# Kernel optimization log

Measured on AMD Instinct MI355X. Metric: run time of the kernel, lower is better.

## Reference

```python
import jax, jax.numpy as jnp
import numpy as np
import math

B, H, W, C = 8, 112, 112, 192
WS, SHIFT, NH = 7, 3, 6
HD = C // NH
N = WS * WS
NW = (H // WS) * (W // WS)
MLP_HID = 4 * C
LOG100 = math.log(100.0)


def _rel_table():
    ch = np.arange(-(WS - 1), WS, dtype=np.float32)
    t = np.stack(np.meshgrid(ch, ch, indexing='ij')).transpose(1, 2, 0).reshape(-1, 2)
    t = t / float(WS - 1) * 8.0
    t = np.sign(t) * np.log2(np.abs(t) + 1.0) / np.log2(8.0)
    return t.astype(np.float32)  # ((2*WS-1)^2, 2)


def _rel_index():
    coords = np.stack(np.meshgrid(np.arange(WS), np.arange(WS), indexing='ij')).reshape(2, -1)
    rel = (coords[:, :, None] - coords[:, None, :]).transpose(1, 2, 0)
    rel = rel + np.array([WS - 1, WS - 1])
    rel = rel * np.array([2 * WS - 1, 1])
    return rel.sum(-1).astype(np.int32)  # (N, N)


def _attn_mask():
    img = np.zeros((H, W), dtype=np.float32)
    cnt = 0
    for hsl in (slice(0, -WS), slice(-WS, -SHIFT), slice(-SHIFT, None)):
        for wsl in (slice(0, -WS), slice(-WS, -SHIFT), slice(-SHIFT, None)):
            img[hsl, wsl] = cnt
            cnt += 1
    mw = img.reshape(H // WS, WS, W // WS, WS).transpose(0, 2, 1, 3).reshape(-1, N)
    diff = mw[:, None, :] - mw[:, :, None]
    return np.where(diff != 0, -100.0, 0.0).astype(np.float32)  # (NW, N, N)

REL_TABLE = jnp.asarray(_rel_table())
REL_INDEX = jnp.asarray(_rel_index())
ATTN_MASK = jnp.asarray(_attn_mask())


def _ln(v, g, b, eps=1e-5):
    m = jnp.mean(v, axis=-1, keepdims=True)
    s = jnp.mean((v - m) ** 2, axis=-1, keepdims=True)
    return (v - m) / jnp.sqrt(s + eps) * g + b


def setup_inputs() -> dict:
    key = jax.random.key(0)
    ks = jax.random.split(key, 12)
    std = 0.02
    inp = {
        'x': jax.random.normal(ks[0], (B, H * W, C), jnp.float32),
        'q_w': jax.random.normal(ks[1], (C, C), jnp.float32) * std,
        'q_b': jnp.zeros((C,), jnp.float32),
        'k_w': jax.random.normal(ks[2], (C, C), jnp.float32) * std,
        'v_w': jax.random.normal(ks[3], (C, C), jnp.float32) * std,
        'v_b': jnp.zeros((C,), jnp.float32),
        'proj_w': jax.random.normal(ks[4], (C, C), jnp.float32) * std,
        'proj_b': jnp.zeros((C,), jnp.float32),
        'logit_scale': jnp.log(10.0 * jnp.ones((NH, 1, 1), jnp.float32)),
        'cpb_w0': jax.random.normal(ks[5], (2, 512), jnp.float32) * std,
        'cpb_b0': jnp.zeros((512,), jnp.float32),
        'cpb_w1': jax.random.normal(ks[6], (512, NH), jnp.float32) * std,
        'ln1_g': jnp.ones((C,), jnp.float32),
        'ln1_b': jnp.zeros((C,), jnp.float32),
        'ln2_g': jnp.ones((C,), jnp.float32),
        'ln2_b': jnp.zeros((C,), jnp.float32),
        'fc1_w': jax.random.normal(ks[7], (C, MLP_HID), jnp.float32) * std,
        'fc1_b': jnp.zeros((MLP_HID,), jnp.float32),
        'fc2_w': jax.random.normal(ks[8], (MLP_HID, C), jnp.float32) * std,
        'fc2_b': jnp.zeros((C,), jnp.float32),
    }
    return inp


def reference(x, q_w, q_b, k_w, v_w, v_b, proj_w, proj_b, logit_scale,
              cpb_w0, cpb_b0, cpb_w1, ln1_g, ln1_b, ln2_g, ln2_b,
              fc1_w, fc1_b, fc2_w, fc2_b):
    shortcut = x  # (B, L, C)
    h = x.reshape(B, H, W, C)
    # cyclic shift
    h = jnp.roll(h, shift=(-SHIFT, -SHIFT), axis=(1, 2))
    # window partition -> (B*NW, N, C)
    h = h.reshape(B, H // WS, WS, W // WS, WS, C).transpose(0, 1, 3, 2, 4, 5)
    h = h.reshape(B * NW, N, C)

    q = (h @ q_w + q_b).reshape(-1, N, NH, HD).transpose(0, 2, 1, 3)
    k = (h @ k_w).reshape(-1, N, NH, HD).transpose(0, 2, 1, 3)
    v = (h @ v_w + v_b).reshape(-1, N, NH, HD).transpose(0, 2, 1, 3)

    # cosine-similarity attention
    q = q / jnp.maximum(jnp.linalg.norm(q, axis=-1, keepdims=True), 1e-6)
    k = k / jnp.maximum(jnp.linalg.norm(k, axis=-1, keepdims=True), 1e-6)
    scale = jnp.exp(jnp.minimum(logit_scale, LOG100))  # (NH,1,1)
    attn = jnp.einsum('bhqd,bhkd->bhqk', q, k) * scale

    # relative position bias via CPB MLP
    rpb = jax.nn.relu(REL_TABLE @ cpb_w0 + cpb_b0) @ cpb_w1  # (169, NH)
    rpb = rpb[REL_INDEX.reshape(-1)].reshape(N, N, NH).transpose(2, 0, 1)
    rpb = 16.0 * jax.nn.sigmoid(rpb)  # (NH, N, N)
    attn = attn + rpb[None]

    # shift mask
    attn = attn.reshape(B, NW, NH, N, N) + ATTN_MASK[None, :, None]
    attn = attn.reshape(B * NW, NH, N, N)
    attn = jax.nn.softmax(attn, axis=-1)

    out = jnp.einsum('bhqk,bhkd->bhqd', attn, v)
    out = out.transpose(0, 2, 1, 3).reshape(B * NW, N, C)
    out = out @ proj_w + proj_b

    # window reverse + reverse shift
    out = out.reshape(B, H // WS, W // WS, WS, WS, C).transpose(0, 1, 3, 2, 4, 5)
    out = out.reshape(B, H, W, C)
    out = jnp.roll(out, shift=(SHIFT, SHIFT), axis=(1, 2)).reshape(B, H * W, C)

    # post-norm residual (Swin-v2)
    h1 = shortcut + _ln(out, ln1_g, ln1_b)
    mlp = jax.nn.gelu(h1 @ fc1_w + fc1_b) @ fc2_w + fc2_b
    return h1 + _ln(mlp, ln2_g, ln2_b)
```

## Files before the change

### kernel.cpp

```cpp
#include <hip/hip_runtime.h>

typedef unsigned short u16;
typedef unsigned int   u32;
typedef __attribute__((ext_vector_type(8))) short bf16x8;
typedef __attribute__((ext_vector_type(4))) float f32x4;

#define B_      8
#define HW_     112
#define C_      192
#define NH_     6
#define HD_     32
#define L_      (HW_*HW_)
#define M_      (B_*L_)
#define MLP_    768
#define QKVN_   576
#define LOG100_ 4.6051702f
#define LOG2E_  1.44269504f

__device__ __forceinline__ float bf2f(u16 u){
  union { float f; u32 i; } v; v.i = ((u32)u) << 16; return v.f;
}
__device__ __forceinline__ u16 f2bf(float f){
  union { float f; u32 i; } v; v.f = f;
  u32 r = (v.i + 0x7fffu + ((v.i >> 16) & 1u)) >> 16;
  return (u16)r;
}
__device__ __forceinline__ u32 cvtpk(float a, float b){
  u32 r;
  asm("v_cvt_pk_bf16_f32 %0, %1, %2" : "=v"(r) : "v"(a), "v"(b));
  return r;
}
__device__ __forceinline__ void u4_to_f8(uint4 u, float* f){
  f[0]=bf2f((u16)(u.x&0xffffu)); f[1]=bf2f((u16)(u.x>>16));
  f[2]=bf2f((u16)(u.y&0xffffu)); f[3]=bf2f((u16)(u.y>>16));
  f[4]=bf2f((u16)(u.z&0xffffu)); f[5]=bf2f((u16)(u.z>>16));
  f[6]=bf2f((u16)(u.w&0xffffu)); f[7]=bf2f((u16)(u.w>>16));
}

__device__ __forceinline__ int rowelem(int b, int wh, int ww, int t){
  int i = t/7, j = t - i*7;
  int oi = wh*7 + i + 3; if (oi >= 112) oi -= 112;
  int oj = ww*7 + j + 3; if (oj >= 112) oj -= 112;
  return b*L_ + oi*112 + oj;
}

__global__ __launch_bounds__(256) void prep_weights(
    const float* __restrict__ qw, const float* __restrict__ qb,
    const float* __restrict__ kw, const float* __restrict__ vw,
    const float* __restrict__ vb, const float* __restrict__ pw,
    const float* __restrict__ pb, const float* __restrict__ f1w,
    const float* __restrict__ f1b, const float* __restrict__ f2w,
    const float* __restrict__ f2b,
    u16* __restrict__ wt_qkv, float* __restrict__ b_qkv,
    u16* __restrict__ wt_p,   float* __restrict__ b_p,
    u16* __restrict__ wt_f1,  float* __restrict__ b_f1,
    u16* __restrict__ wt_f2,  float* __restrict__ b_f2)
{
  const int S1 = 110592, S2 = 147456, S3 = 294912, S4 = 442368, TOT = 444096;
  int i = blockIdx.x*256 + threadIdx.x;
  if (i >= TOT) return;
  if (i < S1) {
    int n = i/192, k = i%192;
    float v = (n<192) ? qw[k*192+n] : ((n<384) ? kw[k*192+(n-192)] : vw[k*192+(n-384)]);
    wt_qkv[i] = f2bf(v);
  } else if (i < S2) {
    int j = i - S1; int n = j/192, k = j%192;
    wt_p[j] = f2bf(pw[k*192+n]);
  } else if (i < S3) {
    int j = i - S2; int n = j/192, k = j%192;
    wt_f1[j] = f2bf(f1w[k*768+n]);
  } else if (i < S4) {
    int j = i - S3; int n = j/768, k = j%768;
    wt_f2[j] = f2bf(f2w[k*192+n]);
  } else {
    int j = i - S4;
    if (j < 576)        b_qkv[j] = (j<192) ? qb[j] : ((j<384) ? 0.f : vb[j-384]);
    else if (j < 768)   b_p[j-576]   = pb[j-576];
    else if (j < 1536)  b_f1[j-768]  = f1b[j-768];
    else                b_f2[j-1536] = f2b[j-1536];
  }
}

__device__ __forceinline__ float reltab(float x){
  float v = x * (8.f/6.f);
  float r = __log2f(fabsf(v) + 1.f) * (1.f/3.f);
  return (v < 0.f) ? -r : r;
}

__global__ __launch_bounds__(64) void rpb_a_kernel(
    const float* __restrict__ w0, const float* __restrict__ b0,
    const float* __restrict__ w1, float* __restrict__ rpb169)
{
  int tt = blockIdx.x, lane = threadIdx.x;
  float t0 = reltab((float)(tt/13 - 6));
  float t1 = reltab((float)(tt%13 - 6));
  float acc[6] = {0.f,0.f,0.f,0.f,0.f,0.f};
  for (int j = lane; j < 512; j += 64){
    float hid = fmaxf(t0*w0[j] + t1*w0[512+j] + b0[j], 0.f);
#pragma unroll
    for (int h=0; h<6; h++) acc[h] += hid * w1[j*6+h];
  }
#pragma unroll
  for (int h=0; h<6; h++){
#pragma unroll
    for (int m=32; m>=1; m>>=1) acc[h] += __shfl_xor(acc[h], m);
  }
  if (lane == 0){
#pragma unroll
    for (int h=0; h<6; h++) rpb169[tt*6+h] = acc[h];
  }
}

__global__ __launch_bounds__(256) void rpb_b_kernel(
    const float* __restrict__ rpb169, float* __restrict__ biasQ)
{
  int i = blockIdx.x*256 + threadIdx.x;
  if (i >= 98304) return;
  int j = i & 63, q = (i >> 6) & 63;
  int rest = i >> 12;
  int hh = rest % 6, type = rest / 6;
  int kt = j >> 4, s = j & 15;
  int key = ((kt>>1)<<5) + ((s>>2)<<3) + ((kt&1)<<2) + (s&3);
  float val;
  if (key >= 49) val = -60000.f;
  else if (q >= 49) val = 0.f;
  else {
    int qi = q/7, qj = q%7, ki = key/7, kj = key%7;
    int idx = (qi - ki + 6)*13 + (qj - kj + 6);
    float x = rpb169[idx*6 + hh];
    float sig = 16.f / (1.f + __expf(-x));
    int th = type >> 1, tw = type & 1;
    int rq = (th ? (qi<4?1:2) : 0)*3 + (tw ? (qj<4?1:2) : 0);
    int rk = (th ? (ki<4?1:2) : 0)*3 + (tw ? (kj<4?1:2) : 0);
    float msk = (rq != rk) ? -100.f : 0.f;
    val = (sig + msk) * LOG2E_;
  }
  biasQ[i] = val;
}

__device__ __forceinline__ float fast_gelu(float v){
  float t = v*v;
  float w = v * fmaf(-0.1029432f, t, -2.30220817f);
  float e = exp2f(w);
  return v * __builtin_amdgcn_rcpf(1.f + e);
}

#define MODE_GELU 0
#define MODE_LN1  1
#define MODE_LN2  2

template<int K, int MODE>
__global__ __launch_bounds__(512,4) void gemm_fused(
    const u16* __restrict__ A, const u16* __restrict__ Wt,
    const float* __restrict__ bias,
    const float* __restrict__ lng, const float* __restrict__ lnb,
    const float* __restrict__ base32, const u16* __restrict__ base16,
    u16* __restrict__ out16, float* __restrict__ out32, int NN)
{
  __shared__ __align__(16) u16 lds[20480];
  const int tid  = threadIdx.x;
  const int wave = tid >> 6, lane = tid & 63;
  const int m0 = blockIdx.x * 128;
  const int n0 = blockIdx.y * 192;
  const int wr = wave >> 1, wc = wave & 1;
  const int lrow = lane >> 2, lslot = lane & 3;
  const int gk = (lslot ^ ((lrow >> 1) & 3)) * 8;

  const u16* gsrc[3]; u32 ldst[3]; const int nst = (wave < 4) ? 3 : 2;
#pragma unroll
  for (int t=0; t<3; t++){
    int c = wave + t*8;
    if (c < 8)       { gsrc[t] = A  + (size_t)(m0 + c*16 + lrow)*K + gk;      ldst[t] = (u32)(c*512); }
    else if (c < 20) { gsrc[t] = Wt + (size_t)(n0 + (c-8)*16 + lrow)*K + gk;  ldst[t] = (u32)(4096 + (c-8)*512); }
    else             { gsrc[t] = A; ldst[t] = 0; }
  }
  const int lr16 = lane & 15;
  const int lg   = lane >> 4;
  const int slot8 = (lg ^ ((lr16 >> 1) & 3)) * 8;
  u32 aoff[2], boff[6];
#pragma unroll
  for (int mt=0; mt<2; mt++) aoff[mt] = (u32)((wr*32 + mt*16 + lr16)*32 + slot8);
#pragma unroll
  for (int nt=0; nt<6; nt++) boff[nt] = (u32)(4096 + (wc*96 + nt*16 + lr16)*32 + slot8);

  f32x4 acc[2][6];
#pragma unroll
  for (int mt=0; mt<2; mt++)
#pragma unroll
    for (int nt=0; nt<6; nt++)
      acc[mt][nt] = (f32x4){0.f,0.f,0.f,0.f};

  const int NT = K/32;
#define STAGE_F(tt, ph) do { \
  _Pragma("unroll") \
  for (int s_=0; s_<3; s_++) if (s_ < nst) \
    __builtin_amdgcn_global_load_lds( \
        (const __attribute__((address_space(1))) void*)(gsrc[s_] + (tt)*32), \
        (__attribute__((address_space(3))) void*)&lds[ldst[s_] + (ph)], 16, 0, 0); \
} while(0)

  STAGE_F(0, 0u);
  __syncthreads();
  for (int t=0; t<NT; t++){
    const u32 pb = (u32)(t&1)*10240u;
    if (t+1 < NT) STAGE_F(t+1, pb ^ 10240u);
    bf16x8 af[2], bf[6];
#pragma unroll
    for (int mt=0; mt<2; mt++) af[mt] = *(const bf16x8*)&lds[pb + aoff[mt]];
#pragma unroll
    for (int nt=0; nt<6; nt++) bf[nt] = *(const bf16x8*)&lds[pb + boff[nt]];
#pragma unroll
    for (int mt=0; mt<2; mt++)
#pragma unroll
      for (int nt=0; nt<6; nt++)
        acc[mt][nt] = __builtin_amdgcn_mfma_f32_16x16x32_bf16(af[mt], bf[nt], acc[mt][nt], 0, 0, 0);
    __syncthreads();
  }
#undef STAGE_F

#pragma unroll
  for (int nt=0; nt<6; nt++){
    float bsv = bias[n0 + wc*96 + nt*16 + lr16];
#pragma unroll
    for (int mt=0; mt<2; mt++)
#pragma unroll
      for (int r2=0; r2<4; r2++) acc[mt][nt][r2] += bsv;
  }

  if (MODE == MODE_GELU){
#pragma unroll
    for (int mt=0; mt<2; mt++){
      int rbase = m0 + wr*32 + mt*16 + lg*4;
#pragma unroll
      for (int nt=0; nt<6; nt++){
        int col = n0 + wc*96 + nt*16 + lr16;
#pragma unroll
        for (int r2=0; r2<4; r2++)
          out16[(size_t)(rbase + r2)*NN + col] = f2bf(fast_gelu(acc[mt][nt][r2]));
      }
    }
  } else {
    float sv[2][4], sq[2][4];
#pragma unroll
    for (int mt=0; mt<2; mt++)
#pragma unroll
      for (int r2=0; r2<4; r2++){
        float s=0.f, q=0.f;
#pragma unroll
        for (int nt=0; nt<6; nt++){ float x = acc[mt][nt][r2]; s += x; q += x*x; }
        sv[mt][r2]=s; sq[mt][r2]=q;
      }
#pragma unroll
    for (int d=1; d<16; d<<=1){
#pragma unroll
      for (int mt=0; mt<2; mt++)
#pragma unroll
        for (int r2=0; r2<4; r2++){
          sv[mt][r2] += __shfl_xor(sv[mt][r2], d);
          sq[mt][r2] += __shfl_xor(sq[mt][r2], d);
        }
    }
    float* red = (float*)lds;
    if (lr16 == 0){
#pragma unroll
      for (int mt=0; mt<2; mt++)
#pragma unroll
        for (int r2=0; r2<4; r2++){
          int row = wr*32 + mt*16 + lg*4 + r2;
          red[row*4 + wc*2]     = sv[mt][r2];
          red[row*4 + wc*2 + 1] = sq[mt][r2];
        }
    }
    __syncthreads();
    float mean[2][4], rstd[2][4];
#pragma unroll
    for (int mt=0; mt<2; mt++)
#pragma unroll
      for (int r2=0; r2<4; r2++){
        int row = wr*32 + mt*16 + lg*4 + r2;
        float s = red[row*4] + red[row*4+2];
        float q = red[row*4+1] + red[row*4+3];
        float m = s*(1.f/192.f);
        float v = fmaxf(q*(1.f/192.f) - m*m, 0.f);
        mean[mt][r2] = m; rstd[mt][r2] = rsqrtf(v + 1e-5f);
      }
    float gg[6], be[6];
#pragma unroll
    for (int nt=0; nt<6; nt++){
      int col = n0 + wc*96 + nt*16 + lr16;
      gg[nt] = lng[col]; be[nt] = lnb[col];
    }
#pragma unroll
    for (int mt=0; mt<2; mt++){
      int rbase = m0 + wr*32 + mt*16 + lg*4;
#pragma unroll
      for (int nt=0; nt<6; nt++){
        int col = n0 + wc*96 + nt*16 + lr16;
#pragma unroll
        for (int r2=0; r2<4; r2++){
          size_t idx = (size_t)(rbase + r2)*192 + col;
          float r = (acc[mt][nt][r2] - mean[mt][r2])*rstd[mt][r2]*gg[nt] + be[nt];
          if (MODE == MODE_LN1){
            r += base32[idx];
            out16[idx] = f2bf(r);
          } else {
            r += bf2f(base16[idx]);
            out32[idx] = r;
          }
        }
      }
    }
  }
}

__global__ __launch_bounds__(512,4) void gemm_qkv_kernel(
    const float* __restrict__ X, const u16* __restrict__ Wt,
    const float* __restrict__ bias, u16* __restrict__ out)
{
  __shared__ __align__(16) u16 lds[20480];
  const int tid  = threadIdx.x;
  const int wave = tid >> 6, lane = tid & 63;
  const int m0 = blockIdx.x * 128;
  const int n0 = blockIdx.y * 192;
  const int wr = wave >> 1, wc = wave & 1;
  const int lrow = lane >> 2, lslot = lane & 3;
  const int gk = (lslot ^ ((lrow >> 1) & 3)) * 8;

  const u16* gsrcB[2]; u32 ldstB[2]; const int nstB = (wave < 4) ? 2 : 1;
#pragma unroll
  for (int t=0; t<2; t++){
    int c = wave + t*8;
    if (c < 12) { gsrcB[t] = Wt + (size_t)(n0 + c*16 + lrow)*192 + gk; ldstB[t] = (u32)(4096 + c*512); }
    else        { gsrcB[t] = Wt; ldstB[t] = 0; }
  }
  const int ar = tid >> 2, as = tid & 3;
  const float* gA = X + (size_t)(m0 + ar)*192 + as*8;
  const u32 dsta = (u32)(ar*32 + (as ^ ((ar >> 1) & 3))*8);

  const int lr16 = lane & 15;
  const int lg   = lane >> 4;
  const int slot8 = (lg ^ ((lr16 >> 1) & 3)) * 8;
  u32 aoff[2], boff[6];
#pragma unroll
  for (int mt=0; mt<2; mt++) aoff[mt] = (u32)((wr*32 + mt*16 + lr16)*32 + slot8);
#pragma unroll
  for (int nt=0; nt<6; nt++) boff[nt] = (u32)(4096 + (wc*96 + nt*16 + lr16)*32 + slot8);

  f32x4 acc[2][6];
#pragma unroll
  for (int mt=0; mt<2; mt++)
#pragma unroll
    for (int nt=0; nt<6; nt++)
      acc[mt][nt] = (f32x4){0.f,0.f,0.f,0.f};

#define STAGE_B(tt, ph) do { \
  _Pragma("unroll") \
  for (int s_=0; s_<2; s_++) if (s_ < nstB) \
    __builtin_amdgcn_global_load_lds( \
        (const __attribute__((address_space(1))) void*)(gsrcB[s_] + (tt)*32), \
        (__attribute__((address_space(3))) void*)&lds[ldstB[s_] + (ph)], 16, 0, 0); \
} while(0)

  {
    float4 a0 = *(const float4*)gA;
    float4 a1 = *(const float4*)(gA + 4);
    STAGE_B(0, 0u);
    uint4 aw;
    aw.x = cvtpk(a0.x, a0.y); aw.y = cvtpk(a0.z, a0.w);
    aw.z = cvtpk(a1.x, a1.y); aw.w = cvtpk(a1.z, a1.w);
    *(uint4*)(void*)&lds[dsta] = aw;
  }
  __syncthreads();

  for (int t=0; t<6; t++){
    const u32 pb = (u32)(t&1)*10240u;
    const u32 pn = pb ^ 10240u;
    float4 a0, a1;
    if (t < 5){
      a0 = *(const float4*)(gA + (t+1)*32);
      a1 = *(const float4*)(gA + (t+1)*32 + 4);
      STAGE_B(t+1, pn);
    }
    bf16x8 af[2], bf[6];
#pragma unroll
    for (int mt=0; mt<2; mt++) af[mt] = *(const bf16x8*)&lds[pb + aoff[mt]];
#pragma unroll
    for (int nt=0; nt<6; nt++) bf[nt] = *(const bf16x8*)&lds[pb + boff[nt]];
#pragma unroll
    for (int mt=0; mt<2; mt++)
#pragma unroll
      for (int nt=0; nt<6; nt++)
        acc[mt][nt] = __builtin_amdgcn_mfma_f32_16x16x32_bf16(af[mt], bf[nt], acc[mt][nt], 0, 0, 0);
    if (t < 5){
      uint4 aw;
      aw.x = cvtpk(a0.x, a0.y); aw.y = cvtpk(a0.z, a0.w);
      aw.z = cvtpk(a1.x, a1.y); aw.w = cvtpk(a1.z, a1.w);
      *(uint4*)(void*)&lds[pn + dsta] = aw;
    }
    __syncthreads();
  }
#undef STAGE_B

#pragma unroll
  for (int mt=0; mt<2; mt++){
    int rbase = m0 + wr*32 + mt*16 + lg*4;
#pragma unroll
    for (int nt=0; nt<6; nt++){
      int col = n0 + wc*96 + nt*16 + lr16;
      float bsv = bias[col];
#pragma unroll
      for (int r2=0; r2<4; r2++)
        out[(size_t)(rbase + r2)*QKVN_ + col] = f2bf(acc[mt][nt][r2] + bsv);
    }
  }
}

__global__ __launch_bounds__(64) void attn_kernel(
    const u16* __restrict__ qkv, const float* __restrict__ lsc,
    const float* __restrict__ biasQ, u16* __restrict__ attn_out)
{
  __shared__ __align__(16) u16 smem[2048];
  char* smb = (char*)smem;
  const int id = blockIdx.x;
  const int hh = id % 6;
  const int w  = id / 6;
  const int b  = w >> 8;
  const int wh = (w >> 4) & 15, ww = w & 15;
  const int lane = threadIdx.x;
  const int lg = lane >> 4, lr = lane & 15;
  const int type = ((wh==15)?2:0) + ((ww==15)?1:0);
  const float qscale = __expf(fminf(lsc[hh], LOG100_)) * LOG2E_;

  union BU { bf16x8 v; u32 u[4]; };

  const int myrow = rowelem(b, wh, ww, min(lane, 48));

  const u16* vsrc = qkv + (size_t)myrow*QKVN_ + 384 + hh*32;
  uint4 vld[4];
#pragma unroll
  for (int r=0; r<4; r++) vld[r] = *(const uint4*)(vsrc + r*8);

  int rowq[4], krow[4];
#pragma unroll
  for (int qt=0; qt<4; qt++) rowq[qt] = __shfl(myrow, qt*16 + lr);
#pragma unroll
  for (int kt=0; kt<4; kt++){
    int sig = ((kt>>1)<<5) + ((lr>>2)<<3) + ((kt&1)<<2) + (lr&3);
    krow[kt] = __shfl(myrow, sig);
  }

  bf16x8 qf[4], kf[4];
#pragma unroll
  for (int qt=0; qt<4; qt++){
    const u16* base = qkv + (size_t)rowq[qt]*QKVN_ + hh*32 + lg*8;
    uint4 u = *(const uint4*)base;
    float f[8]; u4_to_f8(u, f);
    float ss = 0.f;
#pragma unroll
    for (int d=0; d<8; d++) ss += f[d]*f[d];
    ss += __shfl_xor(ss, 16); ss += __shfl_xor(ss, 32);
    float rn = qscale * __builtin_amdgcn_rcpf(fmaxf(sqrtf(ss), 1e-6f));
    BU bu;
#pragma unroll
    for (int p=0; p<4; p++) bu.u[p] = cvtpk(f[2*p]*rn, f[2*p+1]*rn);
    qf[qt] = bu.v;
  }
#pragma unroll
  for (int kt=0; kt<4; kt++){
    const u16* base = qkv + (size_t)krow[kt]*QKVN_ + 192 + hh*32 + lg*8;
    uint4 u = *(const uint4*)base;
    float f[8]; u4_to_f8(u, f);
    float ss = 0.f;
#pragma unroll
    for (int d=0; d<8; d++) ss += f[d]*f[d];
    ss += __shfl_xor(ss, 16); ss += __shfl_xor(ss, 32);
    float rn = __builtin_amdgcn_rcpf(fmaxf(sqrtf(ss), 1e-6f));
    BU bu;
#pragma unroll
    for (int p=0; p<4; p++) bu.u[p] = cvtpk(f[2*p]*rn, f[2*p+1]*rn);
    kf[kt] = bu.v;
  }

  f32x4 s2[4][4];
#pragma unroll
  for (int kt=0; kt<4; kt++)
#pragma unroll
    for (int qt=0; qt<4; qt++)
      s2[kt][qt] = __builtin_amdgcn_mfma_f32_16x16x32_bf16(kf[kt], qf[qt],
                     (f32x4){0.f,0.f,0.f,0.f}, 0, 0, 0);

#pragma unroll
  for (int r=0; r<4; r++){
    u32 wds[4] = {vld[r].x, vld[r].y, vld[r].z, vld[r].w};
#pragma unroll
    for (int i=0; i<8; i++){
      int d = r*8 + i;
      u16 val = (u16)(wds[i>>1] >> ((i&1)*16));
      int addr = (d*128 + lane*2) ^ ((d&7)<<4);
      *(u16*)(smb + addr) = val;
    }
  }

  const float* bq = biasQ + (size_t)(type*6 + hh)*4096;
#pragma unroll
  for (int qt=0; qt<4; qt++){
    int q = qt*16 + lr;
#pragma unroll
    for (int kt=0; kt<4; kt++){
      f32x4 bv = *(const f32x4*)(bq + q*64 + kt*16 + lg*4);
      s2[kt][qt] += bv;
    }
  }
#pragma unroll
  for (int qt=0; qt<4; qt++){
    float m = s2[0][qt][0];
#pragma unroll
    for (int kt=0; kt<4; kt++)
#pragma unroll
      for (int r2=0; r2<4; r2++) m = fmaxf(m, s2[kt][qt][r2]);
    m = fmaxf(m, __shfl_xor(m, 16));
    m = fmaxf(m, __shfl_xor(m, 32));
    float sum = 0.f;
#pragma unroll
    for (int kt=0; kt<4; kt++)
#pragma unroll
      for (int r2=0; r2<4; r2++){
        float e = exp2f(s2[kt][qt][r2] - m);
        s2[kt][qt][r2] = e; sum += e;
      }
    sum += __shfl_xor(sum, 16);
    sum += __shfl_xor(sum, 32);
    float rs = __builtin_amdgcn_rcpf(sum);
#pragma unroll
    for (int kt=0; kt<4; kt++)
#pragma unroll
      for (int r2=0; r2<4; r2++) s2[kt][qt][r2] *= rs;
  }

  __syncthreads();

  f32x4 o2[2][4];
#pragma unroll
  for (int dt=0; dt<2; dt++)
#pragma unroll
    for (int qt=0; qt<4; qt++)
      o2[dt][qt] = (f32x4){0.f,0.f,0.f,0.f};

#pragma unroll
  for (int kb=0; kb<2; kb++){
    bf16x8 af[2];
#pragma unroll
    for (int dt=0; dt<2; dt++){
      int d = dt*16 + lr;
      int addr = (d*128 + kb*64 + lg*16) ^ ((d&7)<<4);
      af[dt] = *(const bf16x8*)(smb + addr);
    }
#pragma unroll
    for (int qt=0; qt<4; qt++){
      BU bu;
      bu.u[0] = cvtpk(s2[2*kb][qt][0],   s2[2*kb][qt][1]);
      bu.u[1] = cvtpk(s2[2*kb][qt][2],   s2[2*kb][qt][3]);
      bu.u[2] = cvtpk(s2[2*kb+1][qt][0], s2[2*kb+1][qt][1]);
      bu.u[3] = cvtpk(s2[2*kb+1][qt][2], s2[2*kb+1][qt][3]);
#pragma unroll
      for (int dt=0; dt<2; dt++)
        o2[dt][qt] = __builtin_amdgcn_mfma_f32_16x16x32_bf16(af[dt], bu.v, o2[dt][qt], 0, 0, 0);
    }
  }

#pragma unroll
  for (int qt=0; qt<4; qt++){
    int q = qt*16 + lr;
    if (q < 49){
      u16* op = attn_out + (size_t)rowq[qt]*C_ + hh*32;
#pragma unroll
      for (int dt=0; dt<2; dt++){
        uint2 u2;
        u2.x = cvtpk(o2[dt][qt][0], o2[dt][qt][1]);
        u2.y = cvtpk(o2[dt][qt][2], o2[dt][qt][3]);
        *(uint2*)(void*)(op + dt*16 + lg*4) = u2;
      }
    }
  }
}

__global__ __launch_bounds__(256,2) void mlp_fused_kernel(
    const u16* __restrict__ h1,
    const u16* __restrict__ wf1,
    const float* __restrict__ bf1,
    const u16* __restrict__ wf2,
    const float* __restrict__ bf2,
    const float* __restrict__ lng, const float* __restrict__ lnb,
    float* __restrict__ out)
{
  __shared__ __align__(16) char smb[75776];
  const int tid  = threadIdx.x;
  const int wave = tid >> 6, lane = tid & 63;
  const int m0 = blockIdx.x * 64;
  const int wr = wave >> 1, wc = wave & 1;
  const int lr16 = lane & 15, lg = lane >> 4;
  const int lrow = lane >> 2, lslot = lane & 3;
  const int gko = (lslot ^ ((lrow >> 1) & 3)) * 8;
  const int slot8 = (lg ^ ((lr16 >> 1) & 3)) * 8;

  {
    const u16* src = h1 + (size_t)m0*192;
#pragma unroll
    for (int j=0; j<6; j++){
      int i = tid + 256*j;
      int row = i/24, c8 = i%24;
      uint4 v = *(const uint4*)(src + i*8);
      *(uint4*)(smb + row*400 + c8*16) = v;
    }
  }

#define STG1(c_, k_, ph_) do { \
  _Pragma("unroll") \
  for (int s_=0; s_<3; s_++){ \
    int ch = wave + s_*4; \
    const u16* sp = wf1 + (size_t)((c_)*192 + ch*16 + lrow)*192 + (k_)*32 + gko; \
    __builtin_amdgcn_global_load_lds( \
        (const __attribute__((address_space(1))) void*)sp, \
        (__attribute__((address_space(3))) void*)(smb + (ph_) + ch*1024), 16, 0, 0); \
  } } while(0)
#define STG2(c_, k_, ph_) do { \
  _Pragma("unroll") \
  for (int s_=0; s_<3; s_++){ \
    int ch = wave + s_*4; \
    const u16* sp = wf2 + (size_t)(ch*16 + lrow)*768 + (c_)*192 + (k_)*32 + gko; \
    __builtin_amdgcn_global_load_lds( \
        (const __attribute__((address_space(1))) void*)sp, \
        (__attribute__((address_space(3))) void*)(smb + (ph_) + ch*1024), 16, 0, 0); \
  } } while(0)

  f32x4 oacc[2][6];
#pragma unroll
  for (int mt=0; mt<2; mt++)
#pragma unroll
    for (int nt=0; nt<6; nt++) oacc[mt][nt] = (f32x4){0.f,0.f,0.f,0.f};

  for (int c=0; c<4; c++){
    f32x4 macc[2][6];
#pragma unroll
    for (int mt=0; mt<2; mt++)
#pragma unroll
      for (int nt=0; nt<6; nt++) macc[mt][nt] = (f32x4){0.f,0.f,0.f,0.f};

    STG1(c, 0, 51200u);
    __syncthreads();
    for (int k=0; k<6; k++){
      u32 pb = 51200u + (u32)(k&1)*12288u;
      if (k < 5) STG1(c, k+1, 51200u + (u32)((k+1)&1)*12288u);
      bf16x8 af[2], bf[6];
#pragma unroll
      for (int mt=0; mt<2; mt++)
        af[mt] = *(const bf16x8*)(smb + ((wr*32 + mt*16 + lr16)*200 + k*32 + lg*8)*2);
#pragma unroll
      for (int nt=0; nt<6; nt++)
        bf[nt] = *(const bf16x8*)(smb + pb + ((wc*96 + nt*16 + lr16)*32 + slot8)*2);
#pragma unroll
      for (int mt=0; mt<2; mt++)
#pragma unroll
        for (int nt=0; nt<6; nt++)
          macc[mt][nt] = __builtin_amdgcn_mfma_f32_16x16x32_bf16(af[mt], bf[nt], macc[mt][nt], 0, 0, 0);
      __syncthreads();
    }
#pragma unroll
    for (int nt=0; nt<6; nt++){
      int col = wc*96 + nt*16 + lr16;
      float bsv = bf1[c*192 + col];
#pragma unroll
      for (int mt=0; mt<2; mt++){
        int row = wr*32 + mt*16 + lg*4;
#pragma unroll
        for (int r2=0; r2<4; r2++){
          float g = fast_gelu(macc[mt][nt][r2] + bsv);
          *(u16*)(smb + 25600 + ((row + r2)*200 + col)*2) = f2bf(g);
        }
      }
    }
    STG2(c, 0, 51200u);
    __syncthreads();
    for (int k=0; k<6; k++){
      u32 pb = 51200u + (u32)(k&1)*12288u;
      if (k < 5) STG2(c, k+1, 51200u + (u32)((k+1)&1)*12288u);
      bf16x8 af[2], bf[6];
#pragma unroll
      for (int mt=0; mt<2; mt++)
        af[mt] = *(const bf16x8*)(smb + 25600 + ((wr*32 + mt*16 + lr16)*200 + k*32 + lg*8)*2);
#pragma unroll
      for (int nt=0; nt<6; nt++)
        bf[nt] = *(const bf16x8*)(smb + pb + ((wc*96 + nt*16 + lr16)*32 + slot8)*2);
#pragma unroll
      for (int mt=0; mt<2; mt++)
#pragma unroll
        for (int nt=0; nt<6; nt++)
          oacc[mt][nt] = __builtin_amdgcn_mfma_f32_16x16x32_bf16(af[mt], bf[nt], oacc[mt][nt], 0, 0, 0);
      __syncthreads();
    }
  }
#undef STG1
#undef STG2

#pragma unroll
  for (int nt=0; nt<6; nt++){
    float bsv = bf2[wc*96 + nt*16 + lr16];
#pragma unroll
    for (int mt=0; mt<2; mt++)
#pragma unroll
      for (int r2=0; r2<4; r2++) oacc[mt][nt][r2] += bsv;
  }
  float sv[2][4], sq[2][4];
#pragma unroll
  for (int mt=0; mt<2; mt++)
#pragma unroll
    for (int r2=0; r2<4; r2++){
      float s=0.f, q=0.f;
#pragma unroll
      for (int nt=0; nt<6; nt++){ float x = oacc[mt][nt][r2]; s += x; q += x*x; }
      sv[mt][r2]=s; sq[mt][r2]=q;
    }
#pragma unroll
  for (int d=1; d<16; d<<=1){
#pragma unroll
    for (int mt=0; mt<2; mt++)
#pragma unroll
      for (int r2=0; r2<4; r2++){
        sv[mt][r2] += __shfl_xor(sv[mt][r2], d);
        sq[mt][r2] += __shfl_xor(sq[mt][r2], d);
      }
  }
  float* red = (float*)(smb + 51200);
  if (lr16 == 0){
#pragma unroll
    for (int mt=0; mt<2; mt++)
#pragma unroll
      for (int r2=0; r2<4; r2++){
        int row = wr*32 + mt*16 + lg*4 + r2;
        red[row*4 + wc*2]     = sv[mt][r2];
        red[row*4 + wc*2 + 1] = sq[mt][r2];
      }
  }
  __syncthreads();
  float gg[6], be[6];
#pragma unroll
  for (int nt=0; nt<6; nt++){
    int col = wc*96 + nt*16 + lr16;
    gg[nt] = lng[col]; be[nt] = lnb[col];
  }
#pragma unroll
  for (int mt=0; mt<2; mt++){
#pragma unroll
    for (int r2=0; r2<4; r2++){
      int row = wr*32 + mt*16 + lg*4 + r2;
      float s = red[row*4] + red[row*4+2];
      float q = red[row*4+1] + red[row*4+3];
      float mean = s*(1.f/192.f);
      float var  = fmaxf(q*(1.f/192.f) - mean*mean, 0.f);
      float rstd = rsqrtf(var + 1e-5f);
#pragma unroll
      for (int nt=0; nt<6; nt++){
        int col = wc*96 + nt*16 + lr16;
        float base = bf2f(*(const u16*)(smb + (row*200 + col)*2));
        float r = base + (oacc[mt][nt][r2] - mean)*rstd*gg[nt] + be[nt];
        out[(size_t)(m0 + row)*192 + col] = r;
      }
    }
  }
}

extern "C" void kernel_launch(void* const* d_in, const int* in_sizes, int n_in,
                              void* d_out, int out_size, void* d_ws, size_t ws_size,
                              hipStream_t stream)
{
  (void)in_sizes; (void)n_in; (void)out_size; (void)ws_size;
  const float* x      = (const float*)d_in[0];
  const float* q_w    = (const float*)d_in[1];
  const float* q_b    = (const float*)d_in[2];
  const float* k_w    = (const float*)d_in[3];
  const float* v_w    = (const float*)d_in[4];
  const float* v_b    = (const float*)d_in[5];
  const float* proj_w = (const float*)d_in[6];
  const float* proj_b = (const float*)d_in[7];
  const float* lsc    = (const float*)d_in[8];
  const float* cpb_w0 = (const float*)d_in[9];
  const float* cpb_b0 = (const float*)d_in[10];
  const float* cpb_w1 = (const float*)d_in[11];
  const float* ln1_g  = (const float*)d_in[12];
  const float* ln1_b  = (const float*)d_in[13];
  const float* ln2_g  = (const float*)d_in[14];
  const float* ln2_b  = (const float*)d_in[15];
  const float* fc1_w  = (const float*)d_in[16];
  const float* fc1_b  = (const float*)d_in[17];
  const float* fc2_w  = (const float*)d_in[18];
  const float* fc2_b  = (const float*)d_in[19];

  char* ws = (char*)d_ws;
  size_t o = 0;
  u16* qkvb = (u16*)(ws + o);    o += 154140672;
  u16* attn_o = (u16*)(ws + o);
  u16* h1b    = attn_o;          o += 38535168;
  u16* wt_qkv = (u16*)(ws + o);  o += 221184;
  float* b_qkv= (float*)(ws + o);o += 2304;
  u16* wt_p   = (u16*)(ws + o);  o += 73728;
  float* b_p  = (float*)(ws + o);o += 768;
  u16* wt_f1  = (u16*)(ws + o);  o += 294912;
  float* b_f1 = (float*)(ws + o);o += 3072;
  u16* wt_f2  = (u16*)(ws + o);  o += 294912;
  float* b_f2 = (float*)(ws + o);o += 768;
  float* rpb169 = (float*)(ws + o); o += 4096;
  float* biasQ  = (float*)(ws + o); o += 393216;

  prep_weights<<<1735, 256, 0, stream>>>(q_w, q_b, k_w, v_w, v_b, proj_w, proj_b,
      fc1_w, fc1_b, fc2_w, fc2_b, wt_qkv, b_qkv, wt_p, b_p, wt_f1, b_f1, wt_f2, b_f2);
  rpb_a_kernel<<<169, 64, 0, stream>>>(cpb_w0, cpb_b0, cpb_w1, rpb169);
  rpb_b_kernel<<<384, 256, 0, stream>>>(rpb169, biasQ);

  gemm_qkv_kernel<<<dim3(784,3), 512, 0, stream>>>(x, wt_qkv, b_qkv, qkvb);
  attn_kernel<<<12288, 64, 0, stream>>>(qkvb, lsc, biasQ, attn_o);
  gemm_fused<192, MODE_LN1><<<dim3(784,1), 512, 0, stream>>>(
      attn_o, wt_p, b_p, ln1_g, ln1_b, x, nullptr, h1b, nullptr, 192);
  mlp_fused_kernel<<<1568, 256, 0, stream>>>(
      h1b, wt_f1, b_f1, wt_f2, b_f2, ln2_g, ln2_b, (float*)d_out);
}
```

Baseline: 328.1 us.

## Flatten MLP fc1/fc2 loops into one pipelined 48-step weight stream

Merges the per-chunk fc1 and fc2 K-loops into a single 48-iteration loop over a unified weight-tile stream. The next tile's global-to-LDS prefetch now continues across the fc1→fc2 and chunk boundaries, which removes the pipeline restarts and extra barriers at each phase change. The fc1 MFMA is transposed (weights as A operand) so each lane holds four consecutive hidden columns. That allows packed bias+GELU and 8-byte bf16 stores to LDS. The cost is runtime branching on r inside the loop and the GELU epilogue sitting inside the pipelined loop.

```diff
diff --git a/kernel.cpp b/kernel.cpp
--- a/kernel.cpp
+++ b/kernel.cpp
@@ -614,93 +614,91 @@
     }
   }
 
-#define STG1(c_, k_, ph_) do { \
+#define BSRC(tt, s_) ({ \
+    int c__ = (tt)/12, r__ = (tt) - c__*12; \
+    int ch__ = wave + (s_)*4; \
+    const u16* p__; \
+    if (r__ < 6) p__ = wf1 + (size_t)((c__*192 + ch__*16 + lrow)*192) + r__*32 + gko; \
+    else         p__ = wf2 + (size_t)((ch__*16 + lrow)*768) + c__*192 + (r__-6)*32 + gko; \
+    p__; })
+#define STGL(tt, ph) do { \
   _Pragma("unroll") \
   for (int s_=0; s_<3; s_++){ \
-    int ch = wave + s_*4; \
-    const u16* sp = wf1 + (size_t)((c_)*192 + ch*16 + lrow)*192 + (k_)*32 + gko; \
+    int ch__ = wave + s_*4; \
     __builtin_amdgcn_global_load_lds( \
-        (const __attribute__((address_space(1))) void*)sp, \
-        (__attribute__((address_space(3))) void*)(smb + (ph_) + ch*1024), 16, 0, 0); \
+        (const __attribute__((address_space(1))) void*)BSRC(tt, s_), \
+        (__attribute__((address_space(3))) void*)(smb + (ph) + ch__*1024), 16, 0, 0); \
   } } while(0)
-#define STG2(c_, k_, ph_) do { \
-  _Pragma("unroll") \
-  for (int s_=0; s_<3; s_++){ \
-    int ch = wave + s_*4; \
-    const u16* sp = wf2 + (size_t)(ch*16 + lrow)*768 + (c_)*192 + (k_)*32 + gko; \
-    __builtin_amdgcn_global_load_lds( \
-        (const __attribute__((address_space(1))) void*)sp, \
-        (__attribute__((address_space(3))) void*)(smb + (ph_) + ch*1024), 16, 0, 0); \
-  } } while(0)
-
+
+  f32x4 macc[6][2];
   f32x4 oacc[2][6];
 #pragma unroll
-  for (int mt=0; mt<2; mt++)
-#pragma unroll
-    for (int nt=0; nt<6; nt++) oacc[mt][nt] = (f32x4){0.f,0.f,0.f,0.f};
-
-  for (int c=0; c<4; c++){
-    f32x4 macc[2][6];
-#pragma unroll
-    for (int mt=0; mt<2; mt++)
-#pragma unroll
-      for (int nt=0; nt<6; nt++) macc[mt][nt] = (f32x4){0.f,0.f,0.f,0.f};
-
-    STG1(c, 0, 51200u);
-    __syncthreads();
-    for (int k=0; k<6; k++){
-      u32 pb = 51200u + (u32)(k&1)*12288u;
-      if (k < 5) STG1(c, k+1, 51200u + (u32)((k+1)&1)*12288u);
-      bf16x8 af[2], bf[6];
+  for (int a=0; a<6; a++)
+#pragma unroll
+    for (int b=0; b<2; b++){ macc[a][b] = (f32x4){0.f,0.f,0.f,0.f}; }
+#pragma unroll
+  for (int a=0; a<2; a++)
+#pragma unroll
+    for (int b=0; b<6; b++){ oacc[a][b] = (f32x4){0.f,0.f,0.f,0.f}; }
+
+  STGL(0, 51200u);
+  __syncthreads();
+
+  for (int tt=0; tt<48; tt++){
+    const int c = tt/12, r = tt - c*12;
+    const u32 pb = 51200u + (u32)(tt&1)*12288u;
+    if (tt+1 < 48) STGL(tt+1, 51200u + (u32)((tt+1)&1)*12288u);
+
+    bf16x8 wfrag[6];
+#pragma unroll
+    for (int nt=0; nt<6; nt++)
+      wfrag[nt] = *(const bf16x8*)(smb + pb + ((wc*96 + nt*16 + lr16)*32 + slot8)*2);
+
+    if (r < 6){
+      bf16x8 af[2];
 #pragma unroll
       for (int mt=0; mt<2; mt++)
-        af[mt] = *(const bf16x8*)(smb + ((wr*32 + mt*16 + lr16)*200 + k*32 + lg*8)*2);
+        af[mt] = *(const bf16x8*)(smb + ((wr*32 + mt*16 + lr16)*200 + r*32 + lg*8)*2);
 #pragma unroll
       for (int nt=0; nt<6; nt++)
-        bf[nt] = *(const bf16x8*)(smb + pb + ((wc*96 + nt*16 + lr16)*32 + slot8)*2);
-#pragma unroll
-      for (int mt=0; mt<2; mt++)
-#pragma unroll
-        for (int nt=0; nt<6; nt++)
-          macc[mt][nt] = __builtin_amdgcn_mfma_f32_16x16x32_bf16(af[mt], bf[nt], macc[mt][nt], 0, 0, 0);
-      __syncthreads();
-    }
-#pragma unroll
-    for (int nt=0; nt<6; nt++){
-      int col = wc*96 + nt*16 + lr16;
-      float bsv = bf1[c*192 + col];
-#pragma unroll
-      for (int mt=0; mt<2; mt++){
-        int row = wr*32 + mt*16 + lg*4;
-#pragma unroll
-        for (int r2=0; r2<4; r2++){
-          float g = fast_gelu(macc[mt][nt][r2] + bsv);
-          *(u16*)(smb + 25600 + ((row + r2)*200 + col)*2) = f2bf(g);
+#pragma unroll
+        for (int mt=0; mt<2; mt++)
+          macc[nt][mt] = __builtin_amdgcn_mfma_f32_16x16x32_bf16(wfrag[nt], af[mt], macc[nt][mt], 0, 0, 0);
+      if (r == 5){
+#pragma unroll
+        for (int nt=0; nt<6; nt++){
+          int colb = wc*96 + nt*16 + lg*4;
+          float b0 = bf1[c*192 + colb],     b1 = bf1[c*192 + colb + 1];
+          float b2 = bf1[c*192 + colb + 2], b3 = bf1[c*192 + colb + 3];
+#pragma unroll
+          for (int mt=0; mt<2; mt++){
+            int tok = wr*32 + mt*16 + lr16;
+            float g0 = fast_gelu(macc[nt][mt][0] + b0);
+            float g1 = fast_gelu(macc[nt][mt][1] + b1);
+            float g2 = fast_gelu(macc[nt][mt][2] + b2);
+            float g3 = fast_gelu(macc[nt][mt][3] + b3);
+            uint2 w; w.x = cvtpk(g0, g1); w.y = cvtpk(g2, g3);
+            *(uint2*)(smb + 25600 + (tok*200 + colb)*2) = w;
+            macc[nt][mt] = (f32x4){0.f,0.f,0.f,0.f};
+          }
         }
       }
-    }
-    STG2(c, 0, 51200u);
-    __syncthreads();
-    for (int k=0; k<6; k++){
-      u32 pb = 51200u + (u32)(k&1)*12288u;
-      if (k < 5) STG2(c, k+1, 51200u + (u32)((k+1)&1)*12288u);
-      bf16x8 af[2], bf[6];
+    } else {
+      const int k = r - 6;
+      bf16x8 af[2];
 #pragma unroll
       for (int mt=0; mt<2; mt++)
         af[mt] = *(const bf16x8*)(smb + 25600 + ((wr*32 + mt*16 + lr16)*200 + k*32 + lg*8)*2);
 #pragma unroll
-      for (int nt=0; nt<6; nt++)
-        bf[nt] = *(const bf16x8*)(smb + pb + ((wc*96 + nt*16 + lr16)*32 + slot8)*2);
-#pragma unroll
       for (int mt=0; mt<2; mt++)
 #pragma unroll
         for (int nt=0; nt<6; nt++)
-          oacc[mt][nt] = __builtin_amdgcn_mfma_f32_16x16x32_bf16(af[mt], bf[nt], oacc[mt][nt], 0, 0, 0);
-      __syncthreads();
-    }
-  }
-#undef STG1
-#undef STG2
+          oacc[mt][nt] = __builtin_amdgcn_mfma_f32_16x16x32_bf16(af[mt], wfrag[nt], oacc[mt][nt], 0, 0, 0);
+    }
+    __syncthreads();
+  }
+#undef STGL
+#undef BSRC
 
 #pragma unroll
   for (int nt=0; nt<6; nt++){
```

Result: no change. 334.0 us (+1.8%).

## Double MLP block to 8 waves with one M-tile each; raise GEMM launch bounds

Applied to the files above, without the earlier changes.

The fused MLP kernel now runs 512 threads per block. Each of the 8 waves owns 16 token rows instead of 32, which halves its accumulator registers and spreads the weight staging over more waves. The second-stage weight prefetch is issued before the GELU epilogue so it can overlap with it. The two GEMM kernels now request 8 blocks per SM in their launch bounds. The higher bounds force the register budget down and may cause spills, and the MLP block still needs 75KB of LDS, which limits how many blocks fit per CU.

```diff
diff --git a/kernel.cpp b/kernel.cpp
--- a/kernel.cpp
+++ b/kernel.cpp
@@ -150,7 +150,7 @@
 #define MODE_LN2  2
 
 template<int K, int MODE>
-__global__ __launch_bounds__(512,4) void gemm_fused(
+__global__ __launch_bounds__(512,8) void gemm_fused(
     const u16* __restrict__ A, const u16* __restrict__ Wt,
     const float* __restrict__ bias,
     const float* __restrict__ lng, const float* __restrict__ lnb,
@@ -313,7 +313,7 @@
   }
 }
 
-__global__ __launch_bounds__(512,4) void gemm_qkv_kernel(
+__global__ __launch_bounds__(512,8) void gemm_qkv_kernel(
     const float* __restrict__ X, const u16* __restrict__ Wt,
     const float* __restrict__ bias, u16* __restrict__ out)
 {
@@ -584,7 +584,7 @@
   }
 }
 
-__global__ __launch_bounds__(256,2) void mlp_fused_kernel(
+__global__ __launch_bounds__(512,4) void mlp_fused_kernel(
     const u16* __restrict__ h1,
     const u16* __restrict__ wf1,
     const float* __restrict__ bf1,
@@ -606,8 +606,8 @@
   {
     const u16* src = h1 + (size_t)m0*192;
 #pragma unroll
-    for (int j=0; j<6; j++){
-      int i = tid + 256*j;
+    for (int j=0; j<3; j++){
+      int i = tid + 512*j;
       int row = i/24, c8 = i%24;
       uint4 v = *(const uint4*)(src + i*8);
       *(uint4*)(smb + row*400 + c8*16) = v;
@@ -616,86 +616,75 @@
 
 #define STG1(c_, k_, ph_) do { \
   _Pragma("unroll") \
-  for (int s_=0; s_<3; s_++){ \
-    int ch = wave + s_*4; \
-    const u16* sp = wf1 + (size_t)((c_)*192 + ch*16 + lrow)*192 + (k_)*32 + gko; \
-    __builtin_amdgcn_global_load_lds( \
-        (const __attribute__((address_space(1))) void*)sp, \
-        (__attribute__((address_space(3))) void*)(smb + (ph_) + ch*1024), 16, 0, 0); \
-  } } while(0)
+  for (int s_=0; s_<2; s_++){ \
+    int ch__ = wave + s_*8; \
+    if (ch__ < 12){ \
+      const u16* sp__ = wf1 + (size_t)((c_)*192 + ch__*16 + lrow)*192 + (k_)*32 + gko; \
+      __builtin_amdgcn_global_load_lds( \
+          (const __attribute__((address_space(1))) void*)sp__, \
+          (__attribute__((address_space(3))) void*)(smb + (ph_) + ch__*1024), 16, 0, 0); \
+    } } } while(0)
 #define STG2(c_, k_, ph_) do { \
   _Pragma("unroll") \
-  for (int s_=0; s_<3; s_++){ \
-    int ch = wave + s_*4; \
-    const u16* sp = wf2 + (size_t)(ch*16 + lrow)*768 + (c_)*192 + (k_)*32 + gko; \
-    __builtin_amdgcn_global_load_lds( \
-        (const __attribute__((address_space(1))) void*)sp, \
-        (__attribute__((address_space(3))) void*)(smb + (ph_) + ch*1024), 16, 0, 0); \
-  } } while(0)
-
-  f32x4 oacc[2][6];
-#pragma unroll
-  for (int mt=0; mt<2; mt++)
-#pragma unroll
-    for (int nt=0; nt<6; nt++) oacc[mt][nt] = (f32x4){0.f,0.f,0.f,0.f};
+  for (int s_=0; s_<2; s_++){ \
+    int ch__ = wave + s_*8; \
+    if (ch__ < 12){ \
+      const u16* sp__ = wf2 + (size_t)(ch__*16 + lrow)*768 + (c_)*192 + (k_)*32 + gko; \
+      __builtin_amdgcn_global_load_lds( \
+          (const __attribute__((address_space(1))) void*)sp__, \
+          (__attribute__((address_space(3))) void*)(smb + (ph_) + ch__*1024), 16, 0, 0); \
+    } } } while(0)
+
+  f32x4 oacc[6];
+#pragma unroll
+  for (int nt=0; nt<6; nt++) oacc[nt] = (f32x4){0.f,0.f,0.f,0.f};
 
   for (int c=0; c<4; c++){
-    f32x4 macc[2][6];
-#pragma unroll
-    for (int mt=0; mt<2; mt++)
-#pragma unroll
-      for (int nt=0; nt<6; nt++) macc[mt][nt] = (f32x4){0.f,0.f,0.f,0.f};
+    f32x4 macc[6];
+#pragma unroll
+    for (int nt=0; nt<6; nt++) macc[nt] = (f32x4){0.f,0.f,0.f,0.f};
 
     STG1(c, 0, 51200u);
     __syncthreads();
+#pragma unroll
     for (int k=0; k<6; k++){
       u32 pb = 51200u + (u32)(k&1)*12288u;
       if (k < 5) STG1(c, k+1, 51200u + (u32)((k+1)&1)*12288u);
-      bf16x8 af[2], bf[6];
-#pragma unroll
-      for (int mt=0; mt<2; mt++)
-        af[mt] = *(const bf16x8*)(smb + ((wr*32 + mt*16 + lr16)*200 + k*32 + lg*8)*2);
+      bf16x8 af = *(const bf16x8*)(smb + ((wr*16 + lr16)*200 + k*32 + lg*8)*2);
+      bf16x8 bfv[6];
 #pragma unroll
       for (int nt=0; nt<6; nt++)
-        bf[nt] = *(const bf16x8*)(smb + pb + ((wc*96 + nt*16 + lr16)*32 + slot8)*2);
-#pragma unroll
-      for (int mt=0; mt<2; mt++)
-#pragma unroll
-        for (int nt=0; nt<6; nt++)
-          macc[mt][nt] = __builtin_amdgcn_mfma_f32_16x16x32_bf16(af[mt], bf[nt], macc[mt][nt], 0, 0, 0);
+        bfv[nt] = *(const bf16x8*)(smb + pb + ((wc*96 + nt*16 + lr16)*32 + slot8)*2);
+#pragma unroll
+      for (int nt=0; nt<6; nt++)
+        macc[nt] = __builtin_amdgcn_mfma_f32_16x16x32_bf16(af, bfv[nt], macc[nt], 0, 0, 0);
       __syncthreads();
     }
+    STG2(c, 0, 51200u);
 #pragma unroll
     for (int nt=0; nt<6; nt++){
       int col = wc*96 + nt*16 + lr16;
       float bsv = bf1[c*192 + col];
 #pragma unroll
-      for (int mt=0; mt<2; mt++){
-        int row = wr*32 + mt*16 + lg*4;
-#pragma unroll
-        for (int r2=0; r2<4; r2++){
-          float g = fast_gelu(macc[mt][nt][r2] + bsv);
-          *(u16*)(smb + 25600 + ((row + r2)*200 + col)*2) = f2bf(g);
-        }
+      for (int r2=0; r2<4; r2++){
+        int tok = wr*16 + lg*4 + r2;
+        float g = fast_gelu(macc[nt][r2] + bsv);
+        *(u16*)(smb + 25600 + (tok*200 + col)*2) = f2bf(g);
       }
     }
-    STG2(c, 0, 51200u);
     __syncthreads();
+#pragma unroll
     for (int k=0; k<6; k++){
       u32 pb = 51200u + (u32)(k&1)*12288u;
       if (k < 5) STG2(c, k+1, 51200u + (u32)((k+1)&1)*12288u);
-      bf16x8 af[2], bf[6];
-#pragma unroll
-      for (int mt=0; mt<2; mt++)
-        af[mt] = *(const bf16x8*)(smb + 25600 + ((wr*32 + mt*16 + lr16)*200 + k*32 + lg*8)*2);
+      bf16x8 af = *(const bf16x8*)(smb + 25600 + ((wr*16 + lr16)*200 + k*32 + lg*8)*2);
+      bf16x8 bfv[6];
 #pragma unroll
       for (int nt=0; nt<6; nt++)
-        bf[nt] = *(const bf16x8*)(smb + pb + ((wc*96 + nt*16 + lr16)*32 + slot8)*2);
-#pragma unroll
-      for (int mt=0; mt<2; mt++)
-#pragma unroll
-        for (int nt=0; nt<6; nt++)
-          oacc[mt][nt] = __builtin_amdgcn_mfma_f32_16x16x32_bf16(af[mt], bf[nt], oacc[mt][nt], 0, 0, 0);
+        bfv[nt] = *(const bf16x8*)(smb + pb + ((wc*96 + nt*16 + lr16)*32 + slot8)*2);
+#pragma unroll
+      for (int nt=0; nt<6; nt++)
+        oacc[nt] = __builtin_amdgcn_mfma_f32_16x16x32_bf16(af, bfv[nt], oacc[nt], 0, 0, 0);
       __syncthreads();
     }
   }
@@ -706,40 +695,32 @@
   for (int nt=0; nt<6; nt++){
     float bsv = bf2[wc*96 + nt*16 + lr16];
 #pragma unroll
-    for (int mt=0; mt<2; mt++)
-#pragma unroll
-      for (int r2=0; r2<4; r2++) oacc[mt][nt][r2] += bsv;
-  }
-  float sv[2][4], sq[2][4];
-#pragma unroll
-  for (int mt=0; mt<2; mt++)
+    for (int r2=0; r2<4; r2++) oacc[nt][r2] += bsv;
+  }
+  float sv[4], sq[4];
+#pragma unroll
+  for (int r2=0; r2<4; r2++){
+    float s=0.f, q=0.f;
+#pragma unroll
+    for (int nt=0; nt<6; nt++){ float x = oacc[nt][r2]; s += x; q += x*x; }
+    sv[r2]=s; sq[r2]=q;
+  }
+#pragma unroll
+  for (int d=1; d<16; d<<=1){
 #pragma unroll
     for (int r2=0; r2<4; r2++){
-      float s=0.f, q=0.f;
-#pragma unroll
-      for (int nt=0; nt<6; nt++){ float x = oacc[mt][nt][r2]; s += x; q += x*x; }
-      sv[mt][r2]=s; sq[mt][r2]=q;
-    }
-#pragma unroll
-  for (int d=1; d<16; d<<=1){
-#pragma unroll
-    for (int mt=0; mt<2; mt++)
-#pragma unroll
-      for (int r2=0; r2<4; r2++){
-        sv[mt][r2] += __shfl_xor(sv[mt][r2], d);
-        sq[mt][r2] += __shfl_xor(sq[mt][r2], d);
-      }
+      sv[r2] += __shfl_xor(sv[r2], d);
+      sq[r2] += __shfl_xor(sq[r2], d);
+    }
   }
   float* red = (float*)(smb + 51200);
   if (lr16 == 0){
 #pragma unroll
-    for (int mt=0; mt<2; mt++)
-#pragma unroll
-      for (int r2=0; r2<4; r2++){
-        int row = wr*32 + mt*16 + lg*4 + r2;
-        red[row*4 + wc*2]     = sv[mt][r2];
-        red[row*4 + wc*2 + 1] = sq[mt][r2];
-      }
+    for (int r2=0; r2<4; r2++){
+      int row = wr*16 + lg*4 + r2;
+      red[row*4 + wc*2]     = sv[r2];
+      red[row*4 + wc*2 + 1] = sq[r2];
+    }
   }
   __syncthreads();
   float gg[6], be[6];
@@ -749,22 +730,18 @@
     gg[nt] = lng[col]; be[nt] = lnb[col];
   }
 #pragma unroll
-  for (int mt=0; mt<2; mt++){
-#pragma unroll
-    for (int r2=0; r2<4; r2++){
-      int row = wr*32 + mt*16 + lg*4 + r2;
-      float s = red[row*4] + red[row*4+2];
-      float q = red[row*4+1] + red[row*4+3];
-      float mean = s*(1.f/192.f);
-      float var  = fmaxf(q*(1.f/192.f) - mean*mean, 0.f);
-      float rstd = rsqrtf(var + 1e-5f);
-#pragma unroll
-      for (int nt=0; nt<6; nt++){
-        int col = wc*96 + nt*16 + lr16;
-        float base = bf2f(*(const u16*)(smb + (row*200 + col)*2));
-        float r = base + (oacc[mt][nt][r2] - mean)*rstd*gg[nt] + be[nt];
-        out[(size_t)(m0 + row)*192 + col] = r;
-      }
+  for (int r2=0; r2<4; r2++){
+    int row = wr*16 + lg*4 + r2;
+    float s = red[row*4] + red[row*4+2];
+    float q = red[row*4+1] + red[row*4+3];
+    float mean = s*(1.f/192.f);
+    float var  = fmaxf(q*(1.f/192.f) - mean*mean, 0.f);
+    float rstd = rsqrtf(var + 1e-5f);
+#pragma unroll
+    for (int nt=0; nt<6; nt++){
+      int col = wc*96 + nt*16 + lr16;
+      float base = bf2f(*(const u16*)(smb + (row*200 + col)*2));
+      out[(size_t)(m0 + row)*192 + col] = base + (oacc[nt][r2] - mean)*rstd*gg[nt] + be[nt];
     }
   }
 }
@@ -820,6 +797,6 @@
   attn_kernel<<<12288, 64, 0, stream>>>(qkvb, lsc, biasQ, attn_o);
   gemm_fused<192, MODE_LN1><<<dim3(784,1), 512, 0, stream>>>(
       attn_o, wt_p, b_p, ln1_g, ln1_b, x, nullptr, h1b, nullptr, 192);
-  mlp_fused_kernel<<<1568, 256, 0, stream>>>(
+  mlp_fused_kernel<<<1568, 512, 0, stream>>>(
       h1b, wt_f1, b_f1, wt_f2, b_f2, ln2_g, ln2_b, (float*)d_out);
 }
```

Result: slower. 821.4 us (+150.3%).
